# Performance work log

Measured on AMD Instinct MI355X. Metric: run time of the kernel, lower is better.

The kernel has to match this reference:

```python
import jax, jax.numpy as jnp
import numpy as np

D_MODEL = 2048
D_INNER = 4096      # expand * d_model
HEADDIM = 64
NHEADS = 64         # d_inner // headdim
D_STATE = 128
NGROUPS = 1
D_CONV = 4
CHUNK = 128
EPS = 1e-5
BATCH = 2
SEQLEN = 4096
D_CONV_CH = D_INNER + 2 * NGROUPS * D_STATE            # 4352
D_IN_PROJ = 2 * D_INNER + 2 * NGROUPS * D_STATE + NHEADS  # 8512


def setup_inputs() -> dict:
    ks = jax.random.split(jax.random.key(0), 9)
    u = jax.random.normal(ks[0], (BATCH, SEQLEN, D_MODEL), jnp.float32)
    W_in = jax.random.normal(ks[1], (D_MODEL, D_IN_PROJ), jnp.float32) * 0.02
    conv_w = jax.random.normal(ks[2], (D_CONV_CH, D_CONV), jnp.float32) * 0.2
    conv_b = jax.random.normal(ks[3], (D_CONV_CH,), jnp.float32) * 0.02
    dt_bias = jax.random.normal(ks[4], (NHEADS,), jnp.float32) * 0.1
    A_log = jax.random.normal(ks[5], (NHEADS,), jnp.float32) * 0.1
    D = jnp.ones((NHEADS,), jnp.float32)
    norm_w = jnp.ones((D_INNER,), jnp.float32)
    W_out = jax.random.normal(ks[8], (D_INNER, D_MODEL), jnp.float32) * 0.02
    return dict(u=u, W_in=W_in, conv_w=conv_w, conv_b=conv_b, dt_bias=dt_bias,
                A_log=A_log, D=D, norm_w=norm_w, W_out=W_out)


def _mamba2_forward(u, W_in, conv_w, conv_b, dt_bias, A_log, D, norm_w, W_out):
    b, L, _ = u.shape
    zxbcdt = u @ W_in                                       # (b, L, 8512)
    z = zxbcdt[..., :D_INNER]
    xBC = zxbcdt[..., D_INNER:D_INNER + D_CONV_CH]
    dt = zxbcdt[..., D_INNER + D_CONV_CH:]                  # (b, L, h)

    # causal depthwise conv1d (padding = d_conv-1, truncated to L) + SiLU
    padded = jnp.pad(xBC, ((0, 0), (D_CONV - 1, 0), (0, 0)))
    xBC_conv = conv_b + sum(padded[:, k:k + L, :] * conv_w[:, k] for k in range(D_CONV))
    xBC_act = jax.nn.silu(xBC_conv)

    x = xBC_act[..., :D_INNER].reshape(b, L, NHEADS, HEADDIM)
    Bm = xBC_act[..., D_INNER:D_INNER + NGROUPS * D_STATE].reshape(b, L, NGROUPS, D_STATE)
    Cm = xBC_act[..., D_INNER + NGROUPS * D_STATE:].reshape(b, L, NGROUPS, D_STATE)
    rep = NHEADS // NGROUPS
    Bh = jnp.repeat(Bm, rep, axis=2)                        # (b, L, h, n)
    Ch = jnp.repeat(Cm, rep, axis=2)

    A = -jnp.exp(A_log)                                     # (h,), negative
    dtf = jax.nn.softplus(dt + dt_bias)                     # (b, L, h)

    # ---- chunked SSD (structured state-space duality) scan ----
    nc = L // CHUNK
    xc = x.reshape(b, nc, CHUNK, NHEADS, HEADDIM)
    Bc = Bh.reshape(b, nc, CHUNK, NHEADS, D_STATE)
    Cc = Ch.reshape(b, nc, CHUNK, NHEADS, D_STATE)
    dtc = dtf.reshape(b, nc, CHUNK, NHEADS)
    cum = jnp.cumsum(dtc * A, axis=2)                       # (b, nc, cs, h), decreasing

    # intra-chunk causal decay matrix L_ij = exp(cum_i - cum_j), i >= j
    idx = jnp.arange(CHUNK)
    mask = (idx[:, None] >= idx[None, :])[None, None, :, :, None]
    seg = cum[:, :, :, None, :] - cum[:, :, None, :, :]     # (b, nc, i, j, h)
    decay = jnp.exp(jnp.where(mask, seg, -jnp.inf))
    CB = jnp.einsum('bcihn,bcjhn->bcijh', Cc, Bc)
    Y_diag = jnp.einsum('bcijh,bcjh,bcjhp->bcihp', CB * decay, dtc, xc)

    # per-chunk final states: sum_j exp(cum_last - cum_j) * dt_j * B_j (x) x_j
    decay_last = jnp.exp(cum[:, :, -1:, :] - cum)           # (b, nc, cs, h)
    states = jnp.einsum('bclh,bclhn,bclhp->bchpn', decay_last * dtc, Bc, xc)

    # inter-chunk recurrence: carry_{c+1} = exp(sum dA_c) * carry_c + states_c
    Atot = jnp.exp(cum[:, :, -1, :])                        # (b, nc, h)
    def step(carry, inp):
        a, s = inp
        return a[..., None, None] * carry + s, carry
    init = jnp.zeros((b, NHEADS, HEADDIM, D_STATE), jnp.float32)
    _, prev = jax.lax.scan(step, init, (jnp.moveaxis(Atot, 1, 0), jnp.moveaxis(states, 1, 0)))
    prev = jnp.moveaxis(prev, 0, 1)                         # (b, nc, h, p, n) state entering each chunk

    Y_off = jnp.einsum('bclhn,bclh,bchpn->bclhp', Cc, jnp.exp(cum), prev)

    y = (Y_diag + Y_off).reshape(b, L, NHEADS, HEADDIM) + D[:, None] * x
    y = y.reshape(b, L, D_INNER)

    # gated RMSNorm: rmsnorm(y * silu(z)) * norm_w
    t = y * jax.nn.silu(z)
    t = t * jax.lax.rsqrt(jnp.mean(t * t, axis=-1, keepdims=True) + EPS) * norm_w
    return t @ W_out


def reference(u, W_in, conv_w, conv_b, dt_bias, A_log, D, norm_w, W_out):
    return _mamba2_forward(u, W_in, conv_w, conv_b, dt_bias, A_log, D, norm_w, W_out)
```

## Files before the change

### kernel.cpp

```cpp
#include <hip/hip_runtime.h>

#define BATCH 2
#define SEQLEN 4096
#define DM 2048
#define DIP 8512
#define DIPP 8576
#define DI 4096
#define DCC 4352
#define NH 64
#define HD 64
#define DSZ 128
#define CHK 128
#define NC 32
#define NBL (BATCH*SEQLEN)
#define LDP 136

typedef __attribute__((ext_vector_type(4))) float f32x4;
typedef __attribute__((ext_vector_type(8))) __bf16 bf16x8;
typedef __attribute__((ext_vector_type(8))) unsigned short us8;
typedef __attribute__((ext_vector_type(4))) unsigned short us4;

__device__ inline float bf2f(unsigned short u){ union{unsigned int i; float f;} v; v.i=((unsigned)u)<<16; return v.f; }
__device__ inline unsigned short f2bf(float f){ union{float f; unsigned int i;} v; v.f=f; unsigned r=(v.i + 0x7FFFu + ((v.i>>16)&1u))>>16; return (unsigned short)r; }

#define GLOAD_LDS16(gp, lp) __builtin_amdgcn_global_load_lds( \
    (const __attribute__((address_space(1))) void*)(gp), \
    (__attribute__((address_space(3))) void*)(lp), 16, 0, 0)

__global__ void beacon_kernel(float* __restrict__ out, float v)
{
    if (blockIdx.x == 0 && threadIdx.x == 0) out[0] = v;
}

__global__ void cast_bf16_kernel(const float* __restrict__ src, unsigned short* __restrict__ dst, size_t n)
{
    size_t stride = (size_t)gridDim.x * blockDim.x * 8;
    for (size_t i = ((size_t)blockIdx.x*blockDim.x + threadIdx.x)*8; i < n; i += stride) {
        float4 a = *(const float4*)&src[i];
        float4 b = *(const float4*)&src[i+4];
        us8 o;
        o[0]=f2bf(a.x); o[1]=f2bf(a.y); o[2]=f2bf(a.z); o[3]=f2bf(a.w);
        o[4]=f2bf(b.x); o[5]=f2bf(b.y); o[6]=f2bf(b.z); o[7]=f2bf(b.w);
        *(us8*)&dst[i] = o;
    }
}

__global__ __launch_bounds__(256) void transpose_cast_kernel(
    const float* __restrict__ in, unsigned short* __restrict__ out, int R, int C)
{
    __shared__ float tile[32][33];
    const int c0 = blockIdx.x*32, r0 = blockIdx.y*32;
    const int tx = threadIdx.x & 31, ty = threadIdx.x >> 5;
    #pragma unroll
    for (int i = 0; i < 4; i++) {
        const int r = r0 + ty + i*8;
        const int c = c0 + tx;
        tile[ty+i*8][tx] = (c < C) ? in[(size_t)r*C + c] : 0.f;
    }
    __syncthreads();
    #pragma unroll
    for (int i = 0; i < 4; i++) {
        const int cc = c0 + ty + i*8;
        const int rr = r0 + tx;
        out[(size_t)cc*R + rr] = f2bf(tile[tx][ty+i*8]);
    }
}

template<int EPI>
__global__ __launch_bounds__(256) void gemm_bt(
    const unsigned short* __restrict__ A, const unsigned short* __restrict__ Bt,
    float* __restrict__ C, int K, int ldc,
    unsigned short* __restrict__ zbf, unsigned short* __restrict__ xbcbf,
    float* __restrict__ dtf, const float* __restrict__ dt_bias)
{
    __shared__ unsigned short As[128*32];
    __shared__ unsigned short Bs[128*32];
    const int m0 = blockIdx.x * 128;
    const int n0 = blockIdx.y * 128;
    const int t = threadIdx.x;
    const int lane = t & 63;
    const int wid = t >> 6;
    const int wr = wid >> 1, wc = wid & 1;

    f32x4 acc[4][4];
    #pragma unroll
    for (int i=0;i<4;i++)
        #pragma unroll
        for (int j=0;j<4;j++) acc[i][j] = f32x4{0.f,0.f,0.f,0.f};

    const int lr = lane & 15;
    const int lkg = (lane >> 4) * 8;

    for (int k0 = 0; k0 < K; k0 += 32) {
        __syncthreads();
        #pragma unroll
        for (int q = 0; q < 2; q++) {
            const int chunk = (wid*2 + q)*64 + lane;
            const int row = chunk >> 2;
            const int ce  = (chunk & 3) * 8;
            GLOAD_LDS16(A  + (size_t)(m0 + row)*K + k0 + ce, &As[(wid*2 + q)*512]);
            GLOAD_LDS16(Bt + (size_t)(n0 + row)*K + k0 + ce, &Bs[(wid*2 + q)*512]);
        }
        __syncthreads();
        bf16x8 af[4], bf[4];
        #pragma unroll
        for (int i=0;i<4;i++) af[i] = *(const bf16x8*)&As[(wr*64 + i*16 + lr)*32 + lkg];
        #pragma unroll
        for (int j=0;j<4;j++) bf[j] = *(const bf16x8*)&Bs[(wc*64 + j*16 + lr)*32 + lkg];
        #pragma unroll
        for (int i=0;i<4;i++)
            #pragma unroll
            for (int j=0;j<4;j++)
                acc[i][j] = __builtin_amdgcn_mfma_f32_16x16x32_bf16(af[i], bf[j], acc[i][j], 0,0,0);
    }
    const int cr = (lane >> 4) * 4;
    const int cc = lane & 15;
    #pragma unroll
    for (int i=0;i<4;i++) {
        #pragma unroll
        for (int j=0;j<4;j++) {
            const int row = m0 + wr*64 + i*16 + cr;
            const int col = n0 + wc*64 + j*16 + cc;
            #pragma unroll
            for (int r=0;r<4;r++) {
                const float val = acc[i][j][r];
                const int rr = row + r;
                if (EPI == 0) {
                    C[(size_t)rr*ldc + col] = val;
                } else {
                    if (col < DI) {
                        zbf[(size_t)rr*DI + col] = f2bf(val);
                    } else if (col < DI + DCC) {
                        xbcbf[(size_t)rr*DCC + (col - DI)] = f2bf(val);
                    } else if (col < DI + DCC + NH) {
                        const int hh = col - (DI + DCC);
                        const float x = val + dt_bias[hh];
                        dtf[(size_t)rr*NH + hh] = (x > 20.f) ? x : log1pf(__expf(x));
                    }
                }
            }
        }
    }
}

__global__ __launch_bounds__(256) void conv_x_kernel(
    const unsigned short* __restrict__ xbc,
    const float* __restrict__ cw, const float* __restrict__ cb,
    unsigned short* __restrict__ xT)
{
    __shared__ float raw[67][68];
    __shared__ unsigned short ot[64][72];
    const int lt = blockIdx.x;
    const int h  = blockIdx.y;
    const int b  = lt >> 6;
    const int l0 = (lt & 63) * 64;
    const int t = threadIdx.x;

    for (int i = t; i < 536; i += 256) {
        const int li = i >> 3, cg = (i & 7) * 8;
        const int l = l0 - 3 + li;
        us8 v;
        #pragma unroll
        for (int e = 0; e < 8; e++) v[e] = 0;
        if (l >= 0) v = *(const us8*)&xbc[(size_t)(b*SEQLEN + l)*DCC + h*64 + cg];
        #pragma unroll
        for (int e = 0; e < 8; e++) raw[li][cg+e] = bf2f(v[e]);
    }
    __syncthreads();
    #pragma unroll
    for (int j = 0; j < 16; j++) {
        const int i = t + j*256;
        const int l = i >> 6, p = i & 63;
        const int ch = h*64 + p;
        float a = cb[ch];
        #pragma unroll
        for (int k = 0; k < 4; k++) a += raw[l + k][p] * cw[ch*4 + k];
        a = a / (1.f + __expf(-a));
        ot[l][p] = f2bf(a);
    }
    __syncthreads();
    for (int i = t; i < 512; i += 256) {
        const int p = i >> 3, lg = (i & 7) * 8;
        us8 o;
        #pragma unroll
        for (int e = 0; e < 8; e++) o[e] = ot[lg + e][p];
        *(us8*)&xT[(size_t)((b*NH + h)*HD + p)*SEQLEN + l0 + lg] = o;
    }
}

__global__ void conv_bc_kernel(const unsigned short* __restrict__ xbc,
                               const float* __restrict__ cw, const float* __restrict__ cb,
                               unsigned short* __restrict__ bcbf)
{
    const int idx = blockIdx.x*256 + threadIdx.x;
    if (idx >= NBL*32) return;
    const int g = idx & 31;
    const int row = idx >> 5;
    const int l = row & (SEQLEN-1);
    const int ch0 = DI + g*8;
    float a[8];
    #pragma unroll
    for (int e=0;e<8;e++) a[e] = cb[ch0+e];
    #pragma unroll
    for (int k = 0; k < 4; k++) {
        if (l + k >= 3) {
            us8 v = *(const us8*)&xbc[(size_t)(row + k - 3)*DCC + ch0];
            #pragma unroll
            for (int e=0;e<8;e++) a[e] += bf2f(v[e]) * cw[(ch0+e)*4 + k];
        }
    }
    us8 o;
    #pragma unroll
    for (int e=0;e<8;e++){ const float s = a[e]/(1.f+__expf(-a[e])); o[e]=f2bf(s); }
    *(us8*)&bcbf[(size_t)row*256 + g*8] = o;
}

__global__ void cum_kernel(const float* __restrict__ dtf, const float* __restrict__ A_log,
                           float* __restrict__ cum)
{
    const int idx = blockIdx.x*256 + threadIdx.x;
    const int h = idx & 63;
    const int bc = idx >> 6;
    const float A = -__expf(A_log[h]);
    float c = 0.f;
    const float* src = dtf + (size_t)bc*CHK*NH + h;
    float* dst = cum + (size_t)bc*CHK*NH + h;
    for (int i = 0; i < CHK; i++) { c += src[i*NH]*A; dst[i*NH] = c; }
}

__global__ __launch_bounds__(256) void ssm_passS(
    const unsigned short* __restrict__ bcbf,
    const unsigned short* __restrict__ xT,
    const float* __restrict__ cumg,
    const float* __restrict__ dtfg,
    unsigned short* __restrict__ states)
{
    __shared__ unsigned short BT[128*LDP];
    __shared__ unsigned short XW[64*LDP];
    __shared__ float cum_s[128], dtc_s[128], w_s[128];

    const int blk = blockIdx.x;
    const int h = blk & 63;
    const int bc = blk >> 6;
    const int r0 = bc * CHK;
    const int t = threadIdx.x;
    const int lane = t & 63;
    const int wid = t >> 6;

    if (t < 128) {
        cum_s[t] = cumg[(size_t)(r0+t)*NH + h];
        dtc_s[t] = dtfg[(size_t)(r0+t)*NH + h];
    }
    for (int i = t; i < 2048; i += 256) {
        const int l = i >> 4, cg = (i & 15)*8;
        us8 v = *(const us8*)(bcbf + (size_t)(r0+l)*256 + cg);
        #pragma unroll
        for (int e = 0; e < 8; e++) BT[(cg+e)*LDP + l] = v[e];
    }
    __syncthreads();
    if (t < 128) w_s[t] = __expf(cum_s[127] - cum_s[t]) * dtc_s[t];
    __syncthreads();
    {
        const int b = bc >> 5;
        const int li = (bc & 31) * CHK;
        const unsigned short* xb = xT + (size_t)((b*NH + h)*HD)*SEQLEN + li;
        for (int i = t; i < 1024; i += 256) {
            const int p = i >> 4, cg = (i & 15)*8;
            us8 v = *(const us8*)(xb + (size_t)p*SEQLEN + cg);
            #pragma unroll
            for (int e = 0; e < 8; e++) v[e] = f2bf(bf2f(v[e]) * w_s[cg+e]);
            *(us8*)&XW[p*LDP + cg] = v;
        }
    }
    __syncthreads();

    const int lr = lane & 15;
    const int lkg = (lane >> 4)*8;
    const int wr = wid >> 1, wc = wid & 1;

    f32x4 acc[2][4];
    #pragma unroll
    for (int i=0;i<2;i++)
        #pragma unroll
        for (int j=0;j<4;j++) acc[i][j] = f32x4{0.f,0.f,0.f,0.f};
    #pragma unroll
    for (int k = 0; k < 4; k++) {
        bf16x8 a[2], b[4];
        #pragma unroll
        for (int i=0;i<2;i++) a[i] = *(const bf16x8*)&XW[(wr*32 + i*16 + lr)*LDP + k*32 + lkg];
        #pragma unroll
        for (int j=0;j<4;j++) b[j] = *(const bf16x8*)&BT[(wc*64 + j*16 + lr)*LDP + k*32 + lkg];
        #pragma unroll
        for (int i=0;i<2;i++)
            #pragma unroll
            for (int j=0;j<4;j++)
                acc[i][j] = __builtin_amdgcn_mfma_f32_16x16x32_bf16(a[i], b[j], acc[i][j], 0,0,0);
    }
    unsigned short* sb = states + (size_t)blk * (HD*DSZ);
    const int cr = (lane >> 4)*4, cc = lane & 15;
    #pragma unroll
    for (int i=0;i<2;i++) {
        #pragma unroll
        for (int j=0;j<4;j++) {
            const int nn = wc*64 + j*16 + cc;
            #pragma unroll
            for (int r=0;r<4;r++) {
                const int pp = wr*32 + i*16 + cr + r;
                sb[pp*DSZ + nn] = f2bf(acc[i][j][r]);
            }
        }
    }
}

__global__ void scan_kernel(unsigned short* __restrict__ states, const float* __restrict__ cumg)
{
    const int idx = blockIdx.x*256 + threadIdx.x;
    const int n = idx & 127;
    const int p = (idx >> 7) & 63;
    const int h = (idx >> 13) & 63;
    const int b = idx >> 19;
    float carry = 0.f;
    for (int c = 0; c < NC; c++) {
        const size_t off = ((size_t)((b*NC + c)*NH + h))*(HD*DSZ) + p*DSZ + n;
        const float s = bf2f(states[off]);
        states[off] = f2bf(carry);
        const float atot = __expf(cumg[(size_t)((b*NC+c)*CHK + 127)*NH + h]);
        carry = atot*carry + s;
    }
}

__global__ __launch_bounds__(256) void ssm_passY(
    const unsigned short* __restrict__ bcbf,
    const unsigned short* __restrict__ xT,
    const unsigned short* __restrict__ statesg,
    const float* __restrict__ cumg,
    const float* __restrict__ dtfg,
    const float* __restrict__ Dg,
    unsigned short* __restrict__ y)
{
    __shared__ unsigned short P1[128*LDP];
    __shared__ unsigned short P2[128*LDP];
    __shared__ unsigned short XTs[64*LDP];
    __shared__ unsigned short PV[64*LDP];
    __shared__ float cum_s[128], dtc_s[128];

    const int blk = blockIdx.x;
    const int h = blk & 63;
    const int bc = blk >> 6;
    const int r0 = bc * CHK;
    const int t = threadIdx.x;
    const int lane = t & 63;
    const int wid = t >> 6;

    if (t < 128) {
        cum_s[t] = cumg[(size_t)(r0+t)*NH + h];
        dtc_s[t] = dtfg[(size_t)(r0+t)*NH + h];
    }
    for (int i = t; i < 2048; i += 256) {
        const int l = i >> 4, cg = (i & 15)*8;
        const unsigned short* src = bcbf + (size_t)(r0+l)*256 + cg;
        *(us8*)&P2[l*LDP + cg] = *(const us8*)src;
        *(us8*)&P1[l*LDP + cg] = *(const us8*)(src + 128);
    }
    {
        const int b = bc >> 5;
        const int li = (bc & 31) * CHK;
        const unsigned short* xb = xT + (size_t)((b*NH + h)*HD)*SEQLEN + li;
        const unsigned short* sb = statesg + (size_t)blk * (HD*DSZ);
        for (int i = t; i < 1024; i += 256) {
            const int p = i >> 4, cg = (i & 15)*8;
            *(us8*)&XTs[p*LDP + cg] = *(const us8*)(xb + (size_t)p*SEQLEN + cg);
            *(us8*)&PV[p*LDP + cg]  = *(const us8*)(sb + p*DSZ + cg);
        }
    }
    __syncthreads();

    const int lr = lane & 15;
    const int lkg = (lane >> 4)*8;
    const int wr = wid >> 1, wc = wid & 1;

    f32x4 acc1[4][4], acc2[4][2];
    #pragma unroll
    for (int i=0;i<4;i++) {
        #pragma unroll
        for (int j=0;j<4;j++) acc1[i][j] = f32x4{0.f,0.f,0.f,0.f};
        #pragma unroll
        for (int j=0;j<2;j++) acc2[i][j] = f32x4{0.f,0.f,0.f,0.f};
    }
    #pragma unroll
    for (int k = 0; k < 4; k++) {
        bf16x8 a[4], b[4], pv[2];
        #pragma unroll
        for (int i=0;i<4;i++) a[i] = *(const bf16x8*)&P1[(wr*64 + i*16 + lr)*LDP + k*32 + lkg];
        #pragma unroll
        for (int j=0;j<4;j++) b[j] = *(const bf16x8*)&P2[(wc*64 + j*16 + lr)*LDP + k*32 + lkg];
        #pragma unroll
        for (int j=0;j<2;j++) pv[j] = *(const bf16x8*)&PV[(wc*32 + j*16 + lr)*LDP + k*32 + lkg];
        #pragma unroll
        for (int i=0;i<4;i++) {
            #pragma unroll
            for (int j=0;j<4;j++)
                acc1[i][j] = __builtin_amdgcn_mfma_f32_16x16x32_bf16(a[i], b[j], acc1[i][j], 0,0,0);
            #pragma unroll
            for (int j=0;j<2;j++)
                acc2[i][j] = __builtin_amdgcn_mfma_f32_16x16x32_bf16(a[i], pv[j], acc2[i][j], 0,0,0);
        }
    }
    __syncthreads();
    const int cr = (lane >> 4)*4, cc = lane & 15;
    #pragma unroll
    for (int i=0;i<4;i++) {
        #pragma unroll
        for (int j=0;j<4;j++) {
            const int jj = wc*64 + j*16 + cc;
            #pragma unroll
            for (int r=0;r<4;r++) {
                const int ii = wr*64 + i*16 + cr + r;
                float v = 0.f;
                if (jj <= ii) v = acc1[i][j][r] * __expf(cum_s[ii] - cum_s[jj]) * dtc_s[jj];
                P1[ii*LDP + jj] = f2bf(v);
            }
        }
    }
    __syncthreads();
    #pragma unroll
    for (int i=0;i<4;i++) {
        #pragma unroll
        for (int r=0;r<4;r++) {
            const int ii = wr*64 + i*16 + cr + r;
            const float sc = __expf(cum_s[ii]);
            #pragma unroll
            for (int j=0;j<2;j++) acc2[i][j][r] *= sc;
        }
    }
    #pragma unroll
    for (int k = 0; k < 4; k++) {
        bf16x8 a[4], x2[2];
        #pragma unroll
        for (int i=0;i<4;i++) a[i] = *(const bf16x8*)&P1[(wr*64 + i*16 + lr)*LDP + k*32 + lkg];
        #pragma unroll
        for (int j=0;j<2;j++) x2[j] = *(const bf16x8*)&XTs[(wc*32 + j*16 + lr)*LDP + k*32 + lkg];
        #pragma unroll
        for (int i=0;i<4;i++)
            #pragma unroll
            for (int j=0;j<2;j++)
                acc2[i][j] = __builtin_amdgcn_mfma_f32_16x16x32_bf16(a[i], x2[j], acc2[i][j], 0,0,0);
    }
    const float Dv = Dg[h];
    #pragma unroll
    for (int i=0;i<4;i++) {
        #pragma unroll
        for (int j=0;j<2;j++) {
            const int pp = wc*32 + j*16 + cc;
            #pragma unroll
            for (int r=0;r<4;r++) {
                const int ii = wr*64 + i*16 + cr + r;
                const float xv = bf2f(XTs[pp*LDP + ii]);
                y[(size_t)(r0+ii)*DI + h*64 + pp] = f2bf(acc2[i][j][r] + Dv * xv);
            }
        }
    }
}

__global__ __launch_bounds__(256) void gate_rms_kernel(
    const unsigned short* __restrict__ y, const unsigned short* __restrict__ z,
    const float* __restrict__ nw, unsigned short* __restrict__ tbf)
{
    const int row = blockIdx.x;
    const int t = threadIdx.x;
    const int lane = t & 63, wid = t >> 6;
    float tv[16];
    float ss = 0.f;
    #pragma unroll
    for (int i = 0; i < 2; i++) {
        const int c = (i*256 + t)*8;
        const us8 yv = *(const us8*)&y[(size_t)row*DI + c];
        const us8 zv = *(const us8*)&z[(size_t)row*DI + c];
        #pragma unroll
        for (int e = 0; e < 8; e++) {
            const float fy = bf2f(yv[e]);
            const float fz = bf2f(zv[e]);
            const float v = fy * (fz / (1.f + __expf(-fz)));
            tv[i*8+e] = v;
            ss += v*v;
        }
    }
    #pragma unroll
    for (int o = 1; o < 64; o <<= 1) ss += __shfl_xor(ss, o, 64);
    __shared__ float red[4];
    if (lane == 0) red[wid] = ss;
    __syncthreads();
    const float rms = rsqrtf((red[0]+red[1]+red[2]+red[3]) * (1.f/DI) + 1e-5f);
    #pragma unroll
    for (int i = 0; i < 2; i++) {
        const int c = (i*256 + t)*8;
        us8 o;
        #pragma unroll
        for (int e = 0; e < 8; e += 4) {
            const float4 wv = *(const float4*)&nw[c + e];
            o[e+0]=f2bf(tv[i*8+e+0]*rms*wv.x);
            o[e+1]=f2bf(tv[i*8+e+1]*rms*wv.y);
            o[e+2]=f2bf(tv[i*8+e+2]*rms*wv.z);
            o[e+3]=f2bf(tv[i*8+e+3]*rms*wv.w);
        }
        *(us8*)&tbf[(size_t)row*DI + c] = o;
    }
}

extern "C" void kernel_launch(void* const* d_in, const int* in_sizes, int n_in,
                              void* d_out, int out_size, void* d_ws, size_t ws_size,
                              hipStream_t stream)
{
    const float* u       = (const float*)d_in[0];
    const float* W_in    = (const float*)d_in[1];
    const float* conv_w  = (const float*)d_in[2];
    const float* conv_b  = (const float*)d_in[3];
    const float* dt_bias = (const float*)d_in[4];
    const float* A_log   = (const float*)d_in[5];
    const float* Dp      = (const float*)d_in[6];
    const float* norm_w  = (const float*)d_in[7];
    const float* W_out   = (const float*)d_in[8];
    float* out = (float*)d_out;

    char* ws = (char*)d_ws;
    const size_t OFF_WINT = 33554432;
    const size_t OFF_R2   = 68681728;
    const size_t OFF_R3   = 139984896;
    const size_t OFF_SM   = 207093760;
    const size_t NEED     = OFF_SM + 2097152 + 2097152 + 4194304;
    if (ws_size < NEED) {
        beacon_kernel<<<1, 64, 0, stream>>>(out, 10000.f + (float)(ws_size >> 20));
        return;
    }

    unsigned short* u_bf   = (unsigned short*)(ws);
    unsigned short* winT   = (unsigned short*)(ws + OFF_WINT);
    unsigned short* xTb    = (unsigned short*)(ws);
    unsigned short* t_bf   = (unsigned short*)(ws);
    unsigned short* xbc_bf = (unsigned short*)(ws + OFF_R2);
    unsigned short* y_bf   = (unsigned short*)(ws + OFF_R2);
    unsigned short* states = (unsigned short*)(ws + OFF_R3);
    unsigned short* woutT  = (unsigned short*)(ws + OFF_R3);
    float*          dtf    = (float*)(ws + OFF_SM);
    float*          cum    = (float*)(ws + OFF_SM + 2097152);
    unsigned short* bc_bf  = (unsigned short*)(ws + OFF_SM + 4194304);
    unsigned short* z_bf   = (unsigned short*)d_out;

    cast_bf16_kernel<<<2048, 256, 0, stream>>>(u, u_bf, (size_t)NBL*DM);
    transpose_cast_kernel<<<dim3(DIPP/32, DM/32), 256, 0, stream>>>(W_in, winT, DM, DIP);
    gemm_bt<1><<<dim3(NBL/128, DIPP/128), 256, 0, stream>>>(
        u_bf, winT, nullptr, DM, 0, z_bf, xbc_bf, dtf, dt_bias);
    conv_x_kernel<<<dim3(NBL/64, NH), 256, 0, stream>>>(xbc_bf, conv_w, conv_b, xTb);
    conv_bc_kernel<<<(NBL*32)/256, 256, 0, stream>>>(xbc_bf, conv_w, conv_b, bc_bf);
    cum_kernel<<<16, 256, 0, stream>>>(dtf, A_log, cum);
    ssm_passS<<<BATCH*NC*NH, 256, 0, stream>>>(bc_bf, xTb, cum, dtf, states);
    scan_kernel<<<4096, 256, 0, stream>>>(states, cum);
    ssm_passY<<<BATCH*NC*NH, 256, 0, stream>>>(bc_bf, xTb, states, cum, dtf, Dp, y_bf);
    gate_rms_kernel<<<NBL, 256, 0, stream>>>(y_bf, z_bf, norm_w, t_bf);
    transpose_cast_kernel<<<dim3(DM/32, DI/32), 256, 0, stream>>>(W_out, woutT, DI, DM);
    gemm_bt<0><<<dim3(NBL/128, DM/128), 256, 0, stream>>>(
        t_bf, woutT, out, DI, DM, nullptr, nullptr, nullptr, nullptr);
}
```

Measured before the change: 1.017 ms.

## Replace GEMM with 256x256 tiled, double-buffered, swizzled-LDS pipelined kernel

Both GEMMs (in-projection and out-projection) switch from a 128x128 tile, single-buffer kernel with two syncs per K step to a 512-thread 256x256 tile kernel. The new kernel uses K=64 steps, double-buffered LDS with XOR-swizzled layout and interleaved global-to-LDS prefetch, plus setprio around MFMA bursts. The aim is to raise arithmetic intensity, hide load latency and avoid LDS bank conflicts. It uses 128KB of LDS and clamps out-of-range B rows for the non-multiple N of the in-projection, which wastes some compute on padded columns.

```diff
diff --git a/kernel.cpp b/kernel.cpp
--- a/kernel.cpp
+++ b/kernel.cpp
@@ -67,60 +67,104 @@
 }
 
 template<int EPI>
-__global__ __launch_bounds__(256) void gemm_bt(
+__global__ __launch_bounds__(512, 2) void gemm256(
     const unsigned short* __restrict__ A, const unsigned short* __restrict__ Bt,
-    float* __restrict__ C, int K, int ldc,
+    float* __restrict__ C, int K, int ldc, int Nmax,
     unsigned short* __restrict__ zbf, unsigned short* __restrict__ xbcbf,
     float* __restrict__ dtf, const float* __restrict__ dt_bias)
 {
-    __shared__ unsigned short As[128*32];
-    __shared__ unsigned short Bs[128*32];
-    const int m0 = blockIdx.x * 128;
-    const int n0 = blockIdx.y * 128;
-    const int t = threadIdx.x;
-    const int lane = t & 63;
-    const int wid = t >> 6;
-    const int wr = wid >> 1, wc = wid & 1;
-
-    f32x4 acc[4][4];
-    #pragma unroll
-    for (int i=0;i<4;i++)
+    __shared__ unsigned short L[65536];
+    const int m0 = blockIdx.x * 256;
+    const int n0 = blockIdx.y * 256;
+    const int tid = threadIdx.x;
+    const int lane = tid & 63;
+    const int wid  = tid >> 6;
+    const int wm = wid >> 2, wn = wid & 3;
+    const int lr  = lane & 15;
+    const int lkg = (lane >> 4) * 8;
+    const int srow = (wid << 4) + (lane >> 3);
+    const int scol = ((lane & 7) ^ (lane >> 3)) << 3;
+    const int cs0 = lkg ^ ((lr & 7) << 3);
+    const int cs1 = cs0 ^ 32;
+    const int nt = K >> 6;
+
+    f32x4 acc[8][4];
+    #pragma unroll
+    for (int i=0;i<8;i++)
         #pragma unroll
         for (int j=0;j<4;j++) acc[i][j] = f32x4{0.f,0.f,0.f,0.f};
 
-    const int lr = lane & 15;
-    const int lkg = (lane >> 4) * 8;
-
-    for (int k0 = 0; k0 < K; k0 += 32) {
-        __syncthreads();
-        #pragma unroll
-        for (int q = 0; q < 2; q++) {
-            const int chunk = (wid*2 + q)*64 + lane;
-            const int row = chunk >> 2;
-            const int ce  = (chunk & 3) * 8;
-            GLOAD_LDS16(A  + (size_t)(m0 + row)*K + k0 + ce, &As[(wid*2 + q)*512]);
-            GLOAD_LDS16(Bt + (size_t)(n0 + row)*K + k0 + ce, &Bs[(wid*2 + q)*512]);
-        }
-        __syncthreads();
-        bf16x8 af[4], bf[4];
-        #pragma unroll
-        for (int i=0;i<4;i++) af[i] = *(const bf16x8*)&As[(wr*64 + i*16 + lr)*32 + lkg];
-        #pragma unroll
-        for (int j=0;j<4;j++) bf[j] = *(const bf16x8*)&Bs[(wc*64 + j*16 + lr)*32 + lkg];
-        #pragma unroll
-        for (int i=0;i<4;i++)
-            #pragma unroll
-            for (int j=0;j<4;j++)
-                acc[i][j] = __builtin_amdgcn_mfma_f32_16x16x32_bf16(af[i], bf[j], acc[i][j], 0,0,0);
-    }
+    auto stA = [&](int buf, int t, int h) {
+        const unsigned short* g = A + (size_t)(m0 + h*128 + srow)*K + t*64 + scol;
+        GLOAD_LDS16(g,               &L[buf*32768 + h*8192 + wid*1024]);
+        GLOAD_LDS16(g + (size_t)8*K, &L[buf*32768 + h*8192 + wid*1024 + 512]);
+    };
+    auto stB = [&](int buf, int t, int h) {
+        const int rr = n0 + h*128 + srow;
+        const int r0 = (rr     > Nmax) ? Nmax : rr;
+        const int r1 = (rr + 8 > Nmax) ? Nmax : rr + 8;
+        GLOAD_LDS16(Bt + (size_t)r0*K + t*64 + scol, &L[buf*32768 + 16384 + h*8192 + wid*1024]);
+        GLOAD_LDS16(Bt + (size_t)r1*K + t*64 + scol, &L[buf*32768 + 16384 + h*8192 + wid*1024 + 512]);
+    };
+
+    bf16x8 bfr[4][2];
+    auto rdA = [&](int buf, int mq, int s, int ks) {
+        const int rl = mq*32 + s*16 + lr;
+        return *(const bf16x8*)&L[buf*32768 + wm*8192 + rl*64 + (ks ? cs1 : cs0)];
+    };
+    auto rdB = [&](int buf, int nf, int ks) {
+        const int rl = (wn & 1)*64 + nf*16 + lr;
+        return *(const bf16x8*)&L[buf*32768 + 16384 + (wn >> 1)*8192 + rl*64 + (ks ? cs1 : cs0)];
+    };
+
+#define PH(BUF, MQ, LOADB, ...) do { \
+    bf16x8 af[2][2]; \
+    af[0][0]=rdA(BUF,MQ,0,0); af[0][1]=rdA(BUF,MQ,0,1); \
+    af[1][0]=rdA(BUF,MQ,1,0); af[1][1]=rdA(BUF,MQ,1,1); \
+    if (LOADB) { \
+        _Pragma("unroll") \
+        for (int nf=0;nf<4;nf++){ bfr[nf][0]=rdB(BUF,nf,0); bfr[nf][1]=rdB(BUF,nf,1);} } \
+    __VA_ARGS__; \
+    asm volatile("s_barrier" ::: "memory"); \
+    __builtin_amdgcn_s_setprio(1); \
+    _Pragma("unroll") \
+    for (int s=0;s<2;s++) { \
+        _Pragma("unroll") \
+        for (int nf=0;nf<4;nf++) { \
+            acc[MQ*2+s][nf] = __builtin_amdgcn_mfma_f32_16x16x32_bf16(af[s][0], bfr[nf][0], acc[MQ*2+s][nf], 0,0,0); \
+            acc[MQ*2+s][nf] = __builtin_amdgcn_mfma_f32_16x16x32_bf16(af[s][1], bfr[nf][1], acc[MQ*2+s][nf], 0,0,0); } } \
+    __builtin_amdgcn_s_setprio(0); \
+    asm volatile("s_barrier" ::: "memory"); \
+} while(0)
+
+    stA(0, 0, 0); stA(0, 0, 1); stB(0, 0, 0); stB(0, 0, 1);
+    stB(1, 1, 0); stB(1, 1, 1);
+    asm volatile("s_waitcnt vmcnt(4)" ::: "memory");
+    asm volatile("s_barrier" ::: "memory");
+
+    #pragma unroll 1
+    for (int t = 0; t < nt; t += 2) {
+        const int tp2 = (t + 2 < nt) ? t + 2 : nt - 1;
+        const int tp3 = (t + 3 < nt) ? t + 3 : nt - 1;
+        PH(0, 0, true,  stA(1, t+1, 0));
+        PH(0, 1, false, stA(1, t+1, 1); stB(0, tp2, 0));
+        PH(0, 2, false, stB(0, tp2, 1));
+        PH(0, 3, false, asm volatile("s_waitcnt vmcnt(4)" ::: "memory"));
+        PH(1, 0, true,  stA(0, tp2, 0));
+        PH(1, 1, false, stA(0, tp2, 1); stB(1, tp3, 0));
+        PH(1, 2, false, stB(1, tp3, 1));
+        PH(1, 3, false, asm volatile("s_waitcnt vmcnt(4)" ::: "memory"));
+    }
+#undef PH
+
     const int cr = (lane >> 4) * 4;
     const int cc = lane & 15;
     #pragma unroll
-    for (int i=0;i<4;i++) {
+    for (int i=0;i<8;i++) {
         #pragma unroll
         for (int j=0;j<4;j++) {
-            const int row = m0 + wr*64 + i*16 + cr;
-            const int col = n0 + wc*64 + j*16 + cc;
+            const int row = m0 + wm*128 + i*16 + cr;
+            const int col = n0 + wn*64 + j*16 + cc;
             #pragma unroll
             for (int r=0;r<4;r++) {
                 const float val = acc[i][j][r];
@@ -548,8 +592,8 @@
 
     cast_bf16_kernel<<<2048, 256, 0, stream>>>(u, u_bf, (size_t)NBL*DM);
     transpose_cast_kernel<<<dim3(DIPP/32, DM/32), 256, 0, stream>>>(W_in, winT, DM, DIP);
-    gemm_bt<1><<<dim3(NBL/128, DIPP/128), 256, 0, stream>>>(
-        u_bf, winT, nullptr, DM, 0, z_bf, xbc_bf, dtf, dt_bias);
+    gemm256<1><<<dim3(NBL/256, (DIPP+255)/256), 512, 0, stream>>>(
+        u_bf, winT, nullptr, DM, 0, DIPP-1, z_bf, xbc_bf, dtf, dt_bias);
     conv_x_kernel<<<dim3(NBL/64, NH), 256, 0, stream>>>(xbc_bf, conv_w, conv_b, xTb);
     conv_bc_kernel<<<(NBL*32)/256, 256, 0, stream>>>(xbc_bf, conv_w, conv_b, bc_bf);
     cum_kernel<<<16, 256, 0, stream>>>(dtf, A_log, cum);
@@ -558,6 +602,6 @@
     ssm_passY<<<BATCH*NC*NH, 256, 0, stream>>>(bc_bf, xTb, states, cum, dtf, Dp, y_bf);
     gate_rms_kernel<<<NBL, 256, 0, stream>>>(y_bf, z_bf, norm_w, t_bf);
     transpose_cast_kernel<<<dim3(DM/32, DI/32), 256, 0, stream>>>(W_out, woutT, DI, DM);
-    gemm_bt<0><<<dim3(NBL/128, DM/128), 256, 0, stream>>>(
-        t_bf, woutT, out, DI, DM, nullptr, nullptr, nullptr, nullptr);
-}
+    gemm256<0><<<dim3(NBL/256, DM/256), 512, 0, stream>>>(
+        t_bf, woutT, out, DI, DM, DM-1, nullptr, nullptr, nullptr, nullptr);
+}
```

Measured after the change: 958.2 us. 5.7% less time.
